# Performance work log

Measured on AMD Instinct MI355X. Metric: run time of the kernel, lower is better.

The kernel has to match this reference:

```python
import jax, jax.numpy as jnp
import numpy as np

Q_DIM = 512
K_DIM = 512
HID = 512


def setup_inputs() -> dict:
    key = jax.random.key(0)
    k1, k2, k3, k4, k5, k6 = jax.random.split(key, 6)
    b, n_q, s = 4, 64, 1024
    queries = jax.random.normal(k1, (b, n_q, Q_DIM), dtype=jnp.float32)
    keys = jax.random.normal(k2, (b, s, K_DIM), dtype=jnp.float32)
    values = jax.random.normal(k3, (b, s, 512), dtype=jnp.float32)
    lim1 = 1.0 / np.sqrt(Q_DIM + K_DIM)
    W1 = jax.random.uniform(k4, (HID, Q_DIM + K_DIM), minval=-lim1, maxval=lim1, dtype=jnp.float32)
    b1 = jax.random.uniform(k5, (HID,), minval=-lim1, maxval=lim1, dtype=jnp.float32)
    lim2 = 1.0 / np.sqrt(HID)
    w2 = jax.random.uniform(k6, (HID,), minval=-lim2, maxval=lim2, dtype=jnp.float32)
    return {"queries": queries, "keys": keys, "values": values,
            "W1": W1, "b1": b1, "w2": w2}


def reference(queries, keys, values, W1, b1, w2):
    # linear1 on concat([q, k]) == W1q @ q + W1k @ k (split the weight),
    # avoiding materializing the concatenated [b, n_q, s, q_v+k_v] tensor.
    W1q = W1[:, :Q_DIM]  # [hid, q_dim]
    W1k = W1[:, Q_DIM:]  # [hid, k_dim]
    q_proj = jnp.einsum('bqd,hd->bqh', queries, W1q)          # [b, n_q, hid]
    k_proj = jnp.einsum('bsd,hd->bsh', keys, W1k) + b1        # [b, s, hid]
    hidden = jnp.tanh(q_proj[:, :, None, :] + k_proj[:, None, :, :])  # [b, n_q, s, hid]
    scores = jnp.einsum('bqsh,h->bqs', hidden, w2)            # [b, n_q, s]
    attn = jax.nn.softmax(scores, axis=2)                     # softmax over key axis
    final = jnp.einsum('bqs,bsv->bqv', attn, values)          # [b, n_q, v_dim]
    return final
```

## Files before the change

### kernel.cpp

```cpp
#include <hip/hip_runtime.h>


static constexpr int SLEN = 1024;
static constexpr int DIM  = 512;
static constexpr float TANH_SCALE = 2.885390081777927f;

typedef __attribute__((ext_vector_type(8))) short bf16x8;
typedef __attribute__((ext_vector_type(4))) float f32x4;

__device__ __forceinline__ float fast_exp2(float x) { return __builtin_amdgcn_exp2f(x); }
__device__ __forceinline__ float fast_rcp(float x)  { return __builtin_amdgcn_rcpf(x); }

__device__ __forceinline__ unsigned int f2bf(float f) {
    unsigned int u = __float_as_uint(f);
    u += 0x7FFF + ((u >> 16) & 1);
    return u >> 16;
}

__device__ __forceinline__ void async_copy16(const void* g, void* l) {
    __builtin_amdgcn_global_load_lds(
        (const __attribute__((address_space(1))) unsigned int*)g,
        (__attribute__((address_space(3))) unsigned int*)l, 16, 0, 0);
}

__global__ __launch_bounds__(256) void convert_bf16(
    const float* __restrict__ q, const float* __restrict__ k,
    const float* __restrict__ w, unsigned short* __restrict__ qb,
    unsigned short* __restrict__ kb, unsigned short* __restrict__ wb)
{
    int id = blockIdx.x * 256 + threadIdx.x;
    const float* src; unsigned short* dst; int off;
    if (id < 32768)        { src = q; dst = qb; off = id; }
    else if (id < 557056)  { src = k; dst = kb; off = id - 32768; }
    else                   { src = w; dst = wb; off = id - 557056; }
    float4 v = ((const float4*)src)[off];
    ushort4 o;
    o.x = (unsigned short)f2bf(v.x); o.y = (unsigned short)f2bf(v.y);
    o.z = (unsigned short)f2bf(v.z); o.w = (unsigned short)f2bf(v.w);
    ((ushort4*)dst)[off] = o;
}

__global__ __launch_bounds__(256) void proj_mfma(
    const unsigned short* __restrict__ qb, const unsigned short* __restrict__ kb,
    const unsigned short* __restrict__ wb, const float* __restrict__ b1,
    float* __restrict__ qp, float* __restrict__ kp)
{
    __shared__ __align__(16) unsigned short As[64][64];
    __shared__ __align__(16) unsigned short Ws[64][64];

    const int bx = blockIdx.x;
    const unsigned short* A; float* C; const float* bias; int mb, nb, col_off;
    if (bx < 512) {
        A = kb; C = kp; bias = b1; col_off = 512;
        mb = (bx >> 3) * 64; nb = (bx & 7) * 64;
    } else {
        int b2 = bx - 512;
        A = qb; C = qp; bias = nullptr; col_off = 0;
        mb = (b2 >> 3) * 64; nb = (b2 & 7) * 64;
    }

    const int t = threadIdx.x;
    const int l = t & 63;
    const int wv = t >> 6;
    const int wm = (wv & 1) * 32;
    const int wn = (wv >> 1) * 32;
    const int lane16 = l & 15;
    const int quad   = l >> 4;
    const int r8   = l >> 3;
    const int schk = (l & 7) ^ r8;

    f32x4 acc[2][2] = {{{0.f,0.f,0.f,0.f},{0.f,0.f,0.f,0.f}},
                       {{0.f,0.f,0.f,0.f},{0.f,0.f,0.f,0.f}}};

    for (int kc = 0; kc < DIM; kc += 64) {
#pragma unroll
        for (int i = 0; i < 2; ++i) {
            int rbase = wv * 16 + i * 8;
            async_copy16(A + (size_t)(mb + rbase + r8) * DIM + kc + schk * 8, &As[rbase][0]);
            async_copy16(wb + (size_t)(nb + rbase + r8) * 1024 + col_off + kc + schk * 8, &Ws[rbase][0]);
        }
        __syncthreads();

#pragma unroll
        for (int ks = 0; ks < 2; ++ks) {
            int cc = ks * 4 + quad;
            int sw = (cc ^ (lane16 & 7)) << 3;
            bf16x8 a0  = *(const bf16x8*)&As[wm + lane16][sw];
            bf16x8 a1  = *(const bf16x8*)&As[wm + 16 + lane16][sw];
            bf16x8 b0  = *(const bf16x8*)&Ws[wn + lane16][sw];
            bf16x8 b1v = *(const bf16x8*)&Ws[wn + 16 + lane16][sw];
            acc[0][0] = __builtin_amdgcn_mfma_f32_16x16x32_bf16(a0, b0,  acc[0][0], 0, 0, 0);
            acc[0][1] = __builtin_amdgcn_mfma_f32_16x16x32_bf16(a0, b1v, acc[0][1], 0, 0, 0);
            acc[1][0] = __builtin_amdgcn_mfma_f32_16x16x32_bf16(a1, b0,  acc[1][0], 0, 0, 0);
            acc[1][1] = __builtin_amdgcn_mfma_f32_16x16x32_bf16(a1, b1v, acc[1][1], 0, 0, 0);
        }
        __syncthreads();
    }

#pragma unroll
    for (int mi = 0; mi < 2; ++mi) {
#pragma unroll
        for (int ni = 0; ni < 2; ++ni) {
            int col = nb + wn + 16 * ni + lane16;
            float bv = bias ? bias[col] : 0.0f;
#pragma unroll
            for (int r = 0; r < 4; ++r) {
                int row = mb + wm + 16 * mi + quad * 4 + r;
                C[(size_t)row * DIM + col] = (acc[mi][ni][r] + bv) * TANH_SCALE;
            }
        }
    }
}

__global__ __launch_bounds__(256) void scores_kernel(
    const float* __restrict__ qp, const float* __restrict__ kp,
    const float* __restrict__ w2, float* __restrict__ th)
{
    __shared__ __align__(16) float qs[16][68];
    __shared__ __align__(16) float ks[32][68];
    __shared__ __align__(16) float ws2[256];
    const int t     = threadIdx.x;
    const int sb    = blockIdx.x * 32;
    const int qt    = blockIdx.y & 3;
    const int half  = blockIdx.y >> 2;
    const int kbase = half * 256;
    const int qrow0 = blockIdx.z * 64 + qt * 16;
    const int krow0 = blockIdx.z * 1024 + sb;
    float* thh = th + (size_t)half * 256 * SLEN;

    if (t < 64) *(float4*)&ws2[t << 2] = *(const float4*)(w2 + kbase + (t << 2));

    const int tq = t >> 4;
    const int ts = t & 15;
    float a00 = 0.f, a01 = 0.f, a10 = 0.f, a11 = 0.f;

    for (int kc = 0; kc < 256; kc += 64) {
        {
            int r = t >> 4, g = (t & 15) << 2;
            *(float4*)&qs[r][g] = *(const float4*)(qp + (size_t)(qrow0 + r) * DIM + kbase + kc + g);
        }
#pragma unroll
        for (int rr = 0; rr < 2; ++rr) {
            int idx = t + rr * 256;
            int r = idx >> 4, g = (idx & 15) << 2;
            *(float4*)&ks[r][g] = *(const float4*)(kp + (size_t)(krow0 + r) * DIM + kbase + kc + g);
        }
        __syncthreads();
#pragma unroll
        for (int k4 = 0; k4 < 16; ++k4) {
            float4 qv = *(const float4*)&qs[tq][k4 << 2];
            float4 k0 = *(const float4*)&ks[ts][k4 << 2];
            float4 k1 = *(const float4*)&ks[ts + 16][k4 << 2];
            float4 wv = *(const float4*)&ws2[kc + (k4 << 2)];
            a00 = fmaf(wv.x, fast_rcp(1.0f + fast_exp2(qv.x + k0.x)), a00);
            a10 = fmaf(wv.x, fast_rcp(1.0f + fast_exp2(qv.x + k1.x)), a10);
            a01 = fmaf(wv.y, fast_rcp(1.0f + fast_exp2(qv.y + k0.y)), a01);
            a11 = fmaf(wv.y, fast_rcp(1.0f + fast_exp2(qv.y + k1.y)), a11);
            a00 = fmaf(wv.z, fast_rcp(1.0f + fast_exp2(qv.z + k0.z)), a00);
            a10 = fmaf(wv.z, fast_rcp(1.0f + fast_exp2(qv.z + k1.z)), a10);
            a01 = fmaf(wv.w, fast_rcp(1.0f + fast_exp2(qv.w + k0.w)), a01);
            a11 = fmaf(wv.w, fast_rcp(1.0f + fast_exp2(qv.w + k1.w)), a11);
        }
        __syncthreads();
    }
    thh[(size_t)(qrow0 + tq) * SLEN + sb + ts]      = a00 + a01;
    thh[(size_t)(qrow0 + tq) * SLEN + sb + ts + 16] = a10 + a11;
}

__global__ __launch_bounds__(256) void combine_kernel(
    const float* __restrict__ th, float* __restrict__ attn)
{
    const int row = blockIdx.x;
    const int t   = threadIdx.x;
    __shared__ float reds[4];
    size_t i0 = (size_t)row * SLEN + (t << 2);
    float4 a = *(const float4*)(th + i0);
    float4 b = *(const float4*)(th + 262144 + i0);
    float4 e;
    e.x = fast_exp2(-TANH_SCALE * (a.x + b.x));
    e.y = fast_exp2(-TANH_SCALE * (a.y + b.y));
    e.z = fast_exp2(-TANH_SCALE * (a.z + b.z));
    e.w = fast_exp2(-TANH_SCALE * (a.w + b.w));
    float s = e.x + e.y + e.z + e.w;
#pragma unroll
    for (int off = 32; off; off >>= 1) s += __shfl_xor(s, off, 64);
    if ((t & 63) == 0) reds[t >> 6] = s;
    __syncthreads();
    s = reds[0] + reds[1] + reds[2] + reds[3];
    float r = fast_rcp(s);
    e.x *= r; e.y *= r; e.z *= r; e.w *= r;
    *(float4*)(attn + i0) = e;
}

__global__ __launch_bounds__(256) void av_gemm(
    const float* __restrict__ attn, const float* __restrict__ values,
    float* __restrict__ pt)
{
    __shared__ __align__(16) float As[32][68];
    __shared__ __align__(16) float Bs[32][68];
    const int t  = threadIdx.x;
    const int nb = blockIdx.x * 64;
    const int kt = blockIdx.y;
    const int kb = kt * 128;
    const int b  = blockIdx.z;
    const int tx = t & 15, ty = t >> 4;
    float acc[4][4] = {};
    for (int kc = 0; kc < 128; kc += 32) {
        const int k0 = kb + kc;
#pragma unroll
        for (int r = 0; r < 2; ++r) {
            int idx = t + r * 256;
            int m   = idx >> 3;
            int k4  = (idx & 7) << 2;
            float4 av = *(const float4*)(attn + (size_t)(b * 64 + m) * SLEN + k0 + k4);
            As[k4 + 0][m] = av.x; As[k4 + 1][m] = av.y;
            As[k4 + 2][m] = av.z; As[k4 + 3][m] = av.w;
            int kk = idx >> 4;
            int g  = (idx & 15) << 2;
            *(float4*)&Bs[kk][g] =
                *(const float4*)(values + (size_t)(b * 1024 + k0 + kk) * DIM + nb + g);
        }
        __syncthreads();
#pragma unroll
        for (int k = 0; k < 32; ++k) {
            float4 a  = *(const float4*)&As[k][ty << 2];
            float4 bv = *(const float4*)&Bs[k][tx << 2];
            float am[4] = {a.x, a.y, a.z, a.w};
            float bn[4] = {bv.x, bv.y, bv.z, bv.w};
#pragma unroll
            for (int i = 0; i < 4; ++i)
#pragma unroll
                for (int j = 0; j < 4; ++j)
                    acc[i][j] = fmaf(am[i], bn[j], acc[i][j]);
        }
        __syncthreads();
    }
#pragma unroll
    for (int i = 0; i < 4; ++i) {
        int row = b * 64 + (ty << 2) + i;
        float4 o;
        o.x = acc[i][0]; o.y = acc[i][1]; o.z = acc[i][2]; o.w = acc[i][3];
        *(float4*)(pt + ((size_t)kt * 256 + row) * DIM + nb + (tx << 2)) = o;
    }
}

__global__ __launch_bounds__(256) void reduce_kernel(
    const float* __restrict__ pt, float* __restrict__ out)
{
    int idx = blockIdx.x * 256 + threadIdx.x;
    const float4* p = (const float4*)pt;
    float4 a = p[idx];
#pragma unroll
    for (int k = 1; k < 8; ++k) {
        float4 v = p[k * 32768 + idx];
        a.x += v.x; a.y += v.y; a.z += v.z; a.w += v.w;
    }
    ((float4*)out)[idx] = a;
}

extern "C" void kernel_launch(void* const* d_in, const int* in_sizes, int n_in,
                              void* d_out, int out_size, void* d_ws, size_t ws_size,
                              hipStream_t stream) {
    const float* queries = (const float*)d_in[0];
    const float* keys    = (const float*)d_in[1];
    const float* values  = (const float*)d_in[2];
    const float* W1      = (const float*)d_in[3];
    const float* b1      = (const float*)d_in[4];
    const float* w2      = (const float*)d_in[5];
    float* out = (float*)d_out;

    float* qp = (float*)d_ws;
    float* kp = qp + 131072;
    float* th = kp + 2097152;
    float* at = th + 2 * 262144;
    float* pt = at + 262144;
    unsigned short* qbf = (unsigned short*)(pt + 8 * 131072);
    unsigned short* kbf = qbf + 131072;
    unsigned short* wbf = kbf + 2097152;
    (void)in_sizes; (void)n_in; (void)ws_size; (void)out_size;

    convert_bf16<<<dim3(2688), 256, 0, stream>>>(queries, keys, W1, qbf, kbf, wbf);
    proj_mfma<<<dim3(544), 256, 0, stream>>>(qbf, kbf, wbf, b1, qp, kp);
    scores_kernel<<<dim3(32, 8, 4), 256, 0, stream>>>(qp, kp, w2, th);
    combine_kernel<<<dim3(256), 256, 0, stream>>>(th, at);
    av_gemm<<<dim3(8, 8, 4), 256, 0, stream>>>(at, values, pt);
    reduce_kernel<<<dim3(128), 256, 0, stream>>>(pt, out);
}
```

Measured before the change: 126.5 us.

## Fuse softmax into AV GEMM and split score reduction into quarters

Removes the separate combine/softmax kernel. The exp of summed partial scores and the row sums now happen while av_gemm loads its tiles, and normalization is deferred to the final reduce kernel. The score kernel is split four ways over the hidden dimension instead of two, doubling its grid to fill more CUs. In exchange, av_gemm redundantly recomputes exp across its 8 column blocks and reads four partial buffers. Softmax max-subtraction is skipped, as before, because tanh bounds the scores.

Result: no change. 128.5 us (+1.6%).

```diff
diff --git a/kernel.cpp b/kernel.cpp
--- a/kernel.cpp
+++ b/kernel.cpp
@@ -118,23 +118,23 @@
 {
     __shared__ __align__(16) float qs[16][68];
     __shared__ __align__(16) float ks[32][68];
-    __shared__ __align__(16) float ws2[256];
+    __shared__ __align__(16) float ws2[128];
     const int t     = threadIdx.x;
     const int sb    = blockIdx.x * 32;
     const int qt    = blockIdx.y & 3;
-    const int half  = blockIdx.y >> 2;
-    const int kbase = half * 256;
+    const int qu    = blockIdx.y >> 2;
+    const int kbase = qu * 128;
     const int qrow0 = blockIdx.z * 64 + qt * 16;
     const int krow0 = blockIdx.z * 1024 + sb;
-    float* thh = th + (size_t)half * 256 * SLEN;
-
-    if (t < 64) *(float4*)&ws2[t << 2] = *(const float4*)(w2 + kbase + (t << 2));
+    float* thh = th + (size_t)qu * 256 * SLEN;
+
+    if (t < 32) *(float4*)&ws2[t << 2] = *(const float4*)(w2 + kbase + (t << 2));
 
     const int tq = t >> 4;
     const int ts = t & 15;
     float a00 = 0.f, a01 = 0.f, a10 = 0.f, a11 = 0.f;
 
-    for (int kc = 0; kc < 256; kc += 64) {
+    for (int kc = 0; kc < 128; kc += 64) {
         {
             int r = t >> 4, g = (t & 15) << 2;
             *(float4*)&qs[r][g] = *(const float4*)(qp + (size_t)(qrow0 + r) * DIM + kbase + kc + g);
@@ -163,38 +163,13 @@
         }
         __syncthreads();
     }
-    thh[(size_t)(qrow0 + tq) * SLEN + sb + ts]      = a00 + a01;
-    thh[(size_t)(qrow0 + tq) * SLEN + sb + ts + 16] = a10 + a11;
-}
-
-__global__ __launch_bounds__(256) void combine_kernel(
-    const float* __restrict__ th, float* __restrict__ attn)
-{
-    const int row = blockIdx.x;
-    const int t   = threadIdx.x;
-    __shared__ float reds[4];
-    size_t i0 = (size_t)row * SLEN + (t << 2);
-    float4 a = *(const float4*)(th + i0);
-    float4 b = *(const float4*)(th + 262144 + i0);
-    float4 e;
-    e.x = fast_exp2(-TANH_SCALE * (a.x + b.x));
-    e.y = fast_exp2(-TANH_SCALE * (a.y + b.y));
-    e.z = fast_exp2(-TANH_SCALE * (a.z + b.z));
-    e.w = fast_exp2(-TANH_SCALE * (a.w + b.w));
-    float s = e.x + e.y + e.z + e.w;
-#pragma unroll
-    for (int off = 32; off; off >>= 1) s += __shfl_xor(s, off, 64);
-    if ((t & 63) == 0) reds[t >> 6] = s;
-    __syncthreads();
-    s = reds[0] + reds[1] + reds[2] + reds[3];
-    float r = fast_rcp(s);
-    e.x *= r; e.y *= r; e.z *= r; e.w *= r;
-    *(float4*)(attn + i0) = e;
+    thh[(size_t)(qrow0 + tq) * SLEN + sb + ts]      = -TANH_SCALE * (a00 + a01);
+    thh[(size_t)(qrow0 + tq) * SLEN + sb + ts + 16] = -TANH_SCALE * (a10 + a11);
 }
 
 __global__ __launch_bounds__(256) void av_gemm(
-    const float* __restrict__ attn, const float* __restrict__ values,
-    float* __restrict__ pt)
+    const float* __restrict__ th, const float* __restrict__ values,
+    float* __restrict__ pt, float* __restrict__ sums_p)
 {
     __shared__ __align__(16) float As[32][68];
     __shared__ __align__(16) float Bs[32][68];
@@ -205,6 +180,7 @@
     const int b  = blockIdx.z;
     const int tx = t & 15, ty = t >> 4;
     float acc[4][4] = {};
+    float rsum[2] = {0.f, 0.f};
     for (int kc = 0; kc < 128; kc += 32) {
         const int k0 = kb + kc;
 #pragma unroll
@@ -212,9 +188,19 @@
             int idx = t + r * 256;
             int m   = idx >> 3;
             int k4  = (idx & 7) << 2;
-            float4 av = *(const float4*)(attn + (size_t)(b * 64 + m) * SLEN + k0 + k4);
-            As[k4 + 0][m] = av.x; As[k4 + 1][m] = av.y;
-            As[k4 + 2][m] = av.z; As[k4 + 3][m] = av.w;
+            size_t base = (size_t)(b * 64 + m) * SLEN + k0 + k4;
+            float4 t0 = *(const float4*)(th + base);
+            float4 t1 = *(const float4*)(th + 262144 + base);
+            float4 t2 = *(const float4*)(th + 524288 + base);
+            float4 t3 = *(const float4*)(th + 786432 + base);
+            float4 e;
+            e.x = fast_exp2(t0.x + t1.x + t2.x + t3.x);
+            e.y = fast_exp2(t0.y + t1.y + t2.y + t3.y);
+            e.z = fast_exp2(t0.z + t1.z + t2.z + t3.z);
+            e.w = fast_exp2(t0.w + t1.w + t2.w + t3.w);
+            As[k4 + 0][m] = e.x; As[k4 + 1][m] = e.y;
+            As[k4 + 2][m] = e.z; As[k4 + 3][m] = e.w;
+            rsum[r] += e.x + e.y + e.z + e.w;
             int kk = idx >> 4;
             int g  = (idx & 15) << 2;
             *(float4*)&Bs[kk][g] =
@@ -242,10 +228,24 @@
         o.x = acc[i][0]; o.y = acc[i][1]; o.z = acc[i][2]; o.w = acc[i][3];
         *(float4*)(pt + ((size_t)kt * 256 + row) * DIM + nb + (tx << 2)) = o;
     }
+    if (nb == 0) {
+#pragma unroll
+        for (int r = 0; r < 2; ++r) {
+            float v = rsum[r];
+            v += __shfl_xor(v, 1, 64);
+            v += __shfl_xor(v, 2, 64);
+            v += __shfl_xor(v, 4, 64);
+            if ((t & 7) == 0) {
+                int m = (t >> 3) + r * 32;
+                sums_p[kt * 256 + b * 64 + m] = v;
+            }
+        }
+    }
 }
 
 __global__ __launch_bounds__(256) void reduce_kernel(
-    const float* __restrict__ pt, float* __restrict__ out)
+    const float* __restrict__ pt, const float* __restrict__ sums_p,
+    float* __restrict__ out)
 {
     int idx = blockIdx.x * 256 + threadIdx.x;
     const float4* p = (const float4*)pt;
@@ -255,6 +255,12 @@
         float4 v = p[k * 32768 + idx];
         a.x += v.x; a.y += v.y; a.z += v.z; a.w += v.w;
     }
+    int row = idx >> 7;
+    float s = 0.f;
+#pragma unroll
+    for (int k = 0; k < 8; ++k) s += sums_p[k * 256 + row];
+    float r = fast_rcp(s);
+    a.x *= r; a.y *= r; a.z *= r; a.w *= r;
     ((float4*)out)[idx] = a;
 }
 
@@ -269,20 +275,19 @@
     const float* w2      = (const float*)d_in[5];
     float* out = (float*)d_out;
 
-    float* qp = (float*)d_ws;
-    float* kp = qp + 131072;
-    float* th = kp + 2097152;
-    float* at = th + 2 * 262144;
-    float* pt = at + 262144;
-    unsigned short* qbf = (unsigned short*)(pt + 8 * 131072);
+    float* qp     = (float*)d_ws;
+    float* kp     = qp + 131072;
+    float* th     = kp + 2097152;
+    float* pt     = th + 4 * 262144;
+    float* sums_p = pt + 8 * 131072;
+    unsigned short* qbf = (unsigned short*)(sums_p + 2048);
     unsigned short* kbf = qbf + 131072;
     unsigned short* wbf = kbf + 2097152;
     (void)in_sizes; (void)n_in; (void)ws_size; (void)out_size;
 
     convert_bf16<<<dim3(2688), 256, 0, stream>>>(queries, keys, W1, qbf, kbf, wbf);
     proj_mfma<<<dim3(544), 256, 0, stream>>>(qbf, kbf, wbf, b1, qp, kp);
-    scores_kernel<<<dim3(32, 8, 4), 256, 0, stream>>>(qp, kp, w2, th);
-    combine_kernel<<<dim3(256), 256, 0, stream>>>(th, at);
-    av_gemm<<<dim3(8, 8, 4), 256, 0, stream>>>(at, values, pt);
-    reduce_kernel<<<dim3(128), 256, 0, stream>>>(pt, out);
-}
+    scores_kernel<<<dim3(32, 16, 4), 256, 0, stream>>>(qp, kp, w2, th);
+    av_gemm<<<dim3(8, 8, 4), 256, 0, stream>>>(th, values, pt, sums_p);
+    reduce_kernel<<<dim3(128), 256, 0, stream>>>(pt, sums_p, out);
+}
```
